# Optimization experiments

Hardware: AMD Instinct MI355X
Metric: run time of the kernel (lower is better)

## Reference

```python
import jax, jax.numpy as jnp
import numpy as np

B, T, D, H, V = 16, 256, 256, 512, 32000  # batch, seq_len, input_dim, hidden, vocab


def setup_inputs() -> dict:
    key = jax.random.key(0)
    ks = jax.random.split(key, 9)
    g = lambda k, shape, scale: (jax.random.normal(k, shape, jnp.float32) * scale)
    return {
        "images": g(ks[0], (B, D), 1.0),
        "labels": jax.random.randint(ks[1], (T, B), 0, V, dtype=jnp.int64),
        "embed_table": g(ks[2], (V, D), 0.02),
        "W_ih": g(ks[3], (4 * H, D), 1.0 / np.sqrt(H)),
        "W_hh": g(ks[4], (4 * H, H), 1.0 / np.sqrt(H)),
        "b_ih": g(ks[5], (4 * H,), 0.01),
        "b_hh": g(ks[6], (4 * H,), 0.01),
        "W_fc": g(ks[7], (V, H), 1.0 / np.sqrt(H)),
        "b_fc": g(ks[8], (V,), 0.01),
    }


def reference(images, labels, embed_table, W_ih, W_hh, b_ih, b_hh, W_fc, b_fc):
    # labels: (T, B) -> embedded (T, B, D); t=0 consumes images instead
    lab_emb = embed_table[labels]                               # (T, B, D)
    x_seq = jnp.concatenate([images[None], lab_emb[1:]], 0)     # (T, B, D)
    # precompute input-side gate contributions for all timesteps (one big GEMM)
    x_gates = jnp.einsum("tbd,gd->tbg", x_seq, W_ih) + b_ih + b_hh  # (T, B, 4H)

    hidden = W_hh.shape[1]
    bsz = images.shape[0]

    def step(carry, xg):
        h, c = carry
        gates = xg + h @ W_hh.T                                 # (B, 4H)
        i, f, g_, o = jnp.split(gates, 4, axis=-1)
        c = jax.nn.sigmoid(f) * c + jax.nn.sigmoid(i) * jnp.tanh(g_)
        h = jax.nn.sigmoid(o) * jnp.tanh(c)
        return (h, c), h

    init = (jnp.zeros((bsz, hidden), x_gates.dtype),
            jnp.zeros((bsz, hidden), x_gates.dtype))
    _, hs = jax.lax.scan(step, init, x_gates)                   # hs: (T, B, H)
    # fc_out applied to every timestep's hidden state
    return jnp.einsum("tbh,vh->tbv", hs, W_fc) + b_fc           # (T, B, V)
```

## Files before the change

kernel.cpp:

```cpp
#include <hip/hip_runtime.h>

typedef __attribute__((ext_vector_type(8))) short short8;
typedef __attribute__((ext_vector_type(4))) float f32x4;
typedef unsigned int uint;
typedef unsigned short ushort;

#define T_ 256
#define B_ 16
#define D_ 256
#define H_ 512
#define V_ 32000
#define GH 2048

__device__ __forceinline__ ushort f2bf(float f) {
    uint u = __float_as_uint(f);
    u += 0x7FFFu + ((u >> 16) & 1u);
    return (ushort)(u >> 16);
}

__device__ __forceinline__ float fsig(float x) {
    return 1.0f / (1.0f + __expf(-x));
}

__device__ __forceinline__ float ftanh(float x) {
    float a = __expf(-2.0f * fabsf(x));
    float t = (1.0f - a) / (1.0f + a);
    return x >= 0.0f ? t : -t;
}

__device__ __forceinline__ void cvt4(const float* s, ushort* d) {
    float4 v = *(const float4*)s;
    ushort4 o;
    o.x = f2bf(v.x); o.y = f2bf(v.y); o.z = f2bf(v.z); o.w = f2bf(v.w);
    *(ushort4*)d = o;
}

__global__ void prep_convert(const float* __restrict__ Wih, const float* __restrict__ Whh,
                             const float* __restrict__ Wfc, const float* __restrict__ bih,
                             const float* __restrict__ bhh,
                             ushort* __restrict__ dWih, ushort* __restrict__ dWhh,
                             ushort* __restrict__ dWfc, float* __restrict__ bsum) {
    const long nA = (long)GH * D_ / 4;
    const long nB = (long)GH * H_ / 4;
    const long nC = (long)V_ * H_ / 4;
    const long nS = GH / 4;
    long i = (long)blockIdx.x * blockDim.x + threadIdx.x;
    if (i >= nA + nB + nC + nS) return;
    if (i < nA) {
        cvt4(Wih + i * 4, dWih + i * 4);
    } else if (i < nA + nB) {
        long j = i - nA;
        cvt4(Whh + j * 4, dWhh + j * 4);
    } else if (i < nA + nB + nC) {
        long j = i - nA - nB;
        cvt4(Wfc + j * 4, dWfc + j * 4);
    } else {
        long j = (i - nA - nB - nC) * 4;
        float4 a = *(const float4*)(bih + j);
        float4 b = *(const float4*)(bhh + j);
        float4 o;
        o.x = a.x + b.x; o.y = a.y + b.y; o.z = a.z + b.z; o.w = a.w + b.w;
        *(float4*)(bsum + j) = o;
    }
}

__global__ void prep_xseq(const float* __restrict__ images, const int* __restrict__ labels,
                          const float* __restrict__ embed, ushort* __restrict__ xseq) {
    int m = blockIdx.x;
    int l = threadIdx.x;
    int t = m >> 4, b = m & 15;
    const float* src = (t == 0) ? (images + b * D_) : (embed + (long)labels[m] * D_);
    cvt4(src + l * 4, xseq + (long)m * D_ + l * 4);
}

template <int K>
__global__ __launch_bounds__(256) void gemm_bt(const ushort* __restrict__ A,
                                               const ushort* __restrict__ Bw,
                                               float* __restrict__ C,
                                               const float* __restrict__ bias,
                                               int ldc) {
    __shared__ ushort As[128 * 64];
    __shared__ ushort Bs[128 * 64];
    const int tid = threadIdx.x;
    const int lane = tid & 63;
    const int w = tid >> 6;
    const int wr = w >> 1, wc = w & 1;
    const long mBase = (long)blockIdx.x * 128;
    const long nBase = (long)blockIdx.y * 128;

    f32x4 acc[4][4];
#pragma unroll
    for (int i = 0; i < 4; ++i)
#pragma unroll
        for (int j = 0; j < 4; ++j) acc[i][j] = (f32x4){0.f, 0.f, 0.f, 0.f};

    const char* Ab = (const char*)A;
    const char* Bb = (const char*)Bw;

    for (int kk = 0; kk < K / 64; ++kk) {
#pragma unroll
        for (int it = 0; it < 4; ++it) {
            int c = w * 4 + it;
            int r = c * 8 + (lane >> 3);
            int sg = (lane & 7) ^ (r & 7);
            long aoff = (mBase + r) * (long)(K * 2) + kk * 128 + sg * 16;
            long boff = (nBase + r) * (long)(K * 2) + kk * 128 + sg * 16;
            __builtin_amdgcn_global_load_lds(
                (const __attribute__((address_space(1))) void*)(Ab + aoff),
                (__attribute__((address_space(3))) void*)((char*)As + c * 1024), 16, 0, 0);
            __builtin_amdgcn_global_load_lds(
                (const __attribute__((address_space(1))) void*)(Bb + boff),
                (__attribute__((address_space(3))) void*)((char*)Bs + c * 1024), 16, 0, 0);
        }
        __syncthreads();
#pragma unroll
        for (int k2 = 0; k2 < 2; ++k2) {
            short8 af[4], bfr[4];
#pragma unroll
            for (int mi = 0; mi < 4; ++mi) {
                int mrow = wr * 64 + mi * 16 + (lane & 15);
                int g = (k2 * 4 + (lane >> 4)) ^ (mrow & 7);
                af[mi] = *(const short8*)((const char*)As + mrow * 128 + g * 16);
            }
#pragma unroll
            for (int ni = 0; ni < 4; ++ni) {
                int nrow = wc * 64 + ni * 16 + (lane & 15);
                int g = (k2 * 4 + (lane >> 4)) ^ (nrow & 7);
                bfr[ni] = *(const short8*)((const char*)Bs + nrow * 128 + g * 16);
            }
#pragma unroll
            for (int mi = 0; mi < 4; ++mi)
#pragma unroll
                for (int ni = 0; ni < 4; ++ni)
                    acc[mi][ni] = __builtin_amdgcn_mfma_f32_16x16x32_bf16(
                        af[mi], bfr[ni], acc[mi][ni], 0, 0, 0);
        }
        __syncthreads();
    }
#pragma unroll
    for (int ni = 0; ni < 4; ++ni) {
        long col = nBase + wc * 64 + ni * 16 + (lane & 15);
        float bv = bias[col];
#pragma unroll
        for (int mi = 0; mi < 4; ++mi) {
            long row0 = mBase + wr * 64 + mi * 16 + ((lane >> 4) << 2);
#pragma unroll
            for (int rr = 0; rr < 4; ++rr)
                C[(row0 + rr) * (long)ldc + col] = acc[mi][ni][rr] + bv;
        }
    }
}

__global__ __launch_bounds__(256) void lstm_scan(const ushort* __restrict__ Whh,
                                                 const float* __restrict__ xg,
                                                 ushort* __restrict__ hs,
                                                 uint* __restrict__ flags) {
    __shared__ ushort Ws[64 * 512];
    __shared__ ushort hb[16 * 512];
    __shared__ float gb[4][16][16];
    __shared__ ushort hloc[16][16];

    const int tid = threadIdx.x;
    const int lane = tid & 63;
    const int w = tid >> 6;
    const int g = blockIdx.x;

#pragma unroll
    for (int j = 0; j < 16; ++j) {
        int gid = j * 256 + tid;
        int row = gid >> 6;
        int gcol = gid & 63;
        int srow = (row >> 4) * H_ + g * 16 + (row & 15);
        uint4 v = *(const uint4*)(Whh + (long)srow * H_ + gcol * 8);
        int dg = gcol ^ (row & 7);
        *(uint4*)((char*)Ws + row * 1024 + dg * 16) = v;
    }
    __syncthreads();

    const int b = tid >> 4;
    const int jj = tid & 15;
    float cst = 0.0f;

    for (int t = 0; t < T_; ++t) {
        long xb = ((long)t * B_ + b) * GH + g * 16 + jj;
        float gi = xg[xb];
        float gf = xg[xb + 512];
        float gg = xg[xb + 1024];
        float go = xg[xb + 1536];

        if (t > 0) {
            int fi = lane & 31;
            uint v = __hip_atomic_load(&flags[fi], __ATOMIC_RELAXED, __HIP_MEMORY_SCOPE_AGENT);
            int guard = 0;
            while (v < (uint)t) {
                __builtin_amdgcn_s_sleep(1);
                v = __hip_atomic_load(&flags[fi], __ATOMIC_RELAXED, __HIP_MEMORY_SCOPE_AGENT);
                if (++guard > (1 << 20)) break;
            }
            const uint* hsrcU = (const uint*)hs + ((long)(t - 1) * (B_ * H_)) / 2;
            const int row = tid >> 4;
            const int c0 = tid & 15;
            uint vals[16];
#pragma unroll
            for (int j2 = 0; j2 < 16; ++j2)
                vals[j2] = __hip_atomic_load((uint*)(hsrcU + row * 256 + c0 + j2 * 16),
                                             __ATOMIC_RELAXED, __HIP_MEMORY_SCOPE_AGENT);
#pragma unroll
            for (int j2 = 0; j2 < 16; ++j2) {
                int u = c0 + j2 * 16;
                int gcol = u >> 2, sub = u & 3;
                int dg = gcol ^ (row & 7);
                *(uint*)((char*)hb + row * 1024 + dg * 16 + sub * 4) = vals[j2];
            }
            __syncthreads();
            f32x4 acc0 = (f32x4){0.f, 0.f, 0.f, 0.f};
            f32x4 acc1 = (f32x4){0.f, 0.f, 0.f, 0.f};
            const int arow = lane & 15;
            const int brow = w * 16 + (lane & 15);
#pragma unroll
            for (int k0 = 0; k0 < 16; k0 += 2) {
                int ga0 = (k0 * 4 + (lane >> 4)) ^ (arow & 7);
                int gB0 = (k0 * 4 + (lane >> 4)) ^ (brow & 7);
                int ga1 = ((k0 + 1) * 4 + (lane >> 4)) ^ (arow & 7);
                int gB1 = ((k0 + 1) * 4 + (lane >> 4)) ^ (brow & 7);
                short8 a0 = *(const short8*)((const char*)hb + arow * 1024 + ga0 * 16);
                short8 b0 = *(const short8*)((const char*)Ws + brow * 1024 + gB0 * 16);
                short8 a1 = *(const short8*)((const char*)hb + arow * 1024 + ga1 * 16);
                short8 b1 = *(const short8*)((const char*)Ws + brow * 1024 + gB1 * 16);
                acc0 = __builtin_amdgcn_mfma_f32_16x16x32_bf16(a0, b0, acc0, 0, 0, 0);
                acc1 = __builtin_amdgcn_mfma_f32_16x16x32_bf16(a1, b1, acc1, 0, 0, 0);
            }
#pragma unroll
            for (int r = 0; r < 4; ++r)
                gb[w][((lane >> 4) << 2) + r][lane & 15] = acc0[r] + acc1[r];
            __syncthreads();
            gi += gb[0][b][jj];
            gf += gb[1][b][jj];
            gg += gb[2][b][jj];
            go += gb[3][b][jj];
        }
        float ii = fsig(gi), ff = fsig(gf), oo = fsig(go), tg = ftanh(gg);
        cst = ff * cst + ii * tg;
        float hv = oo * ftanh(cst);
        hloc[b][jj] = f2bf(hv);
        __syncthreads();
        if (tid < 128) {
            int bb = tid >> 3, u = tid & 7;
            uint val = (uint)hloc[bb][u * 2] | ((uint)hloc[bb][u * 2 + 1] << 16);
            uint* dst = (uint*)hs + (((long)t * B_ + bb) * H_ + g * 16) / 2 + u;
            __hip_atomic_store(dst, val, __ATOMIC_RELAXED, __HIP_MEMORY_SCOPE_AGENT);
        }
        asm volatile("s_waitcnt vmcnt(0)" ::: "memory");
        __syncthreads();
        if (tid == 0)
            __hip_atomic_store(&flags[g], (uint)(t + 1), __ATOMIC_RELAXED, __HIP_MEMORY_SCOPE_AGENT);
    }
}

extern "C" void kernel_launch(void* const* d_in, const int* in_sizes, int n_in,
                              void* d_out, int out_size, void* d_ws, size_t ws_size,
                              hipStream_t stream) {
    const float* images = (const float*)d_in[0];
    const int* labels   = (const int*)d_in[1];
    const float* embed  = (const float*)d_in[2];
    const float* Wih    = (const float*)d_in[3];
    const float* Whh    = (const float*)d_in[4];
    const float* bih    = (const float*)d_in[5];
    const float* bhh    = (const float*)d_in[6];
    const float* Wfc    = (const float*)d_in[7];
    const float* bfc    = (const float*)d_in[8];
    float* out = (float*)d_out;

    char* p = (char*)d_ws;
    ushort* dWfc = (ushort*)p; p += (long)V_ * H_ * 2;
    ushort* dWih = (ushort*)p; p += (long)GH * D_ * 2;
    ushort* dWhh = (ushort*)p; p += (long)GH * H_ * 2;
    ushort* xseq = (ushort*)p; p += (long)T_ * B_ * D_ * 2;
    float* xg    = (float*)p;  p += (long)T_ * B_ * GH * 4;
    ushort* hs   = (ushort*)p; p += (long)T_ * B_ * H_ * 2;
    float* bsum  = (float*)p;  p += GH * 4;
    uint* flags  = (uint*)p;   p += 256;

    hipMemsetAsync(flags, 0, 32 * sizeof(uint), stream);

    {
        long total = (long)GH * D_ / 4 + (long)GH * H_ / 4 + (long)V_ * H_ / 4 + GH / 4;
        int blocks = (int)((total + 255) / 256);
        prep_convert<<<blocks, 256, 0, stream>>>(Wih, Whh, Wfc, bih, bhh, dWih, dWhh, dWfc, bsum);
    }
    prep_xseq<<<T_ * B_, 64, 0, stream>>>(images, labels, embed, xseq);

    gemm_bt<D_><<<dim3(32, 16), 256, 0, stream>>>(xseq, dWih, xg, bsum, GH);

    lstm_scan<<<32, 256, 0, stream>>>(dWhh, xg, hs, flags);

    gemm_bt<H_><<<dim3(32, 250), 256, 0, stream>>>(hs, dWfc, out, bfc, V_);
}
```

Baseline: 1.031 ms.

## Replace per-step flag barrier with sentinel-valued hidden-state polling

The inter-block flag array is replaced by pre-filling the hidden-state buffer with a 0xFFFFFFFF sentinel. Each block now polls the previous step's h values directly until none are sentinel, and takes its own slice from shared memory. Writers store packed bf16 pairs straight from registers via a lane shuffle, which removes the vmcnt wait, one __syncthreads and the flag store on each step. This shortens the per-step serial critical path of the 256-step recurrence. The cost is a 4 MB memset, and correctness relies on no real bf16 pair ever equalling the sentinel, which holds because 0xFFFF is a NaN pattern.

New measurement: 897.4 us. -12.9%, faster.

```diff
diff --git a/kernel.cpp b/kernel.cpp
--- a/kernel.cpp
+++ b/kernel.cpp
@@ -11,6 +11,7 @@
 #define H_ 512
 #define V_ 32000
 #define GH 2048
+#define SENT 0xFFFFFFFFu
 
 __device__ __forceinline__ ushort f2bf(float f) {
     uint u = __float_as_uint(f);
@@ -153,8 +154,7 @@
 
 __global__ __launch_bounds__(256) void lstm_scan(const ushort* __restrict__ Whh,
                                                  const float* __restrict__ xg,
-                                                 ushort* __restrict__ hs,
-                                                 uint* __restrict__ flags) {
+                                                 ushort* __restrict__ hs) {
     __shared__ ushort Ws[64 * 512];
     __shared__ ushort hb[16 * 512];
     __shared__ float gb[4][16][16];
@@ -179,6 +179,8 @@
 
     const int b = tid >> 4;
     const int jj = tid & 15;
+    const int row = tid >> 4;
+    const int c0 = tid & 15;
     float cst = 0.0f;
 
     for (int t = 0; t < T_; ++t) {
@@ -189,28 +191,36 @@
         float go = xg[xb + 1536];
 
         if (t > 0) {
-            int fi = lane & 31;
-            uint v = __hip_atomic_load(&flags[fi], __ATOMIC_RELAXED, __HIP_MEMORY_SCOPE_AGENT);
+            uint vals[16];
+#pragma unroll
+            for (int j = 0; j < 16; ++j) {
+                int u = c0 + j * 16;
+                if ((u >> 3) == g)
+                    vals[j] = (uint)hloc[row][(u & 7) * 2] |
+                              ((uint)hloc[row][(u & 7) * 2 + 1] << 16);
+                else
+                    vals[j] = SENT;
+            }
+            uint* hsrcU = (uint*)hs + ((long)(t - 1) * (B_ * H_)) / 2 + row * 256;
             int guard = 0;
-            while (v < (uint)t) {
-                __builtin_amdgcn_s_sleep(1);
-                v = __hip_atomic_load(&flags[fi], __ATOMIC_RELAXED, __HIP_MEMORY_SCOPE_AGENT);
-                if (++guard > (1 << 20)) break;
-            }
-            const uint* hsrcU = (const uint*)hs + ((long)(t - 1) * (B_ * H_)) / 2;
-            const int row = tid >> 4;
-            const int c0 = tid & 15;
-            uint vals[16];
-#pragma unroll
-            for (int j2 = 0; j2 < 16; ++j2)
-                vals[j2] = __hip_atomic_load((uint*)(hsrcU + row * 256 + c0 + j2 * 16),
-                                             __ATOMIC_RELAXED, __HIP_MEMORY_SCOPE_AGENT);
-#pragma unroll
-            for (int j2 = 0; j2 < 16; ++j2) {
-                int u = c0 + j2 * 16;
+            for (;;) {
+                int pend = 0;
+#pragma unroll
+                for (int j = 0; j < 16; ++j) {
+                    if (vals[j] == SENT)
+                        vals[j] = __hip_atomic_load(hsrcU + c0 + j * 16,
+                                                    __ATOMIC_RELAXED, __HIP_MEMORY_SCOPE_AGENT);
+                }
+#pragma unroll
+                for (int j = 0; j < 16; ++j) pend += (vals[j] == SENT) ? 1 : 0;
+                if (pend == 0 || ++guard > (1 << 20)) break;
+            }
+#pragma unroll
+            for (int j = 0; j < 16; ++j) {
+                int u = c0 + j * 16;
                 int gcol = u >> 2, sub = u & 3;
                 int dg = gcol ^ (row & 7);
-                *(uint*)((char*)hb + row * 1024 + dg * 16 + sub * 4) = vals[j2];
+                *(uint*)((char*)hb + row * 1024 + dg * 16 + sub * 4) = vals[j];
             }
             __syncthreads();
             f32x4 acc0 = (f32x4){0.f, 0.f, 0.f, 0.f};
@@ -242,18 +252,16 @@
         float ii = fsig(gi), ff = fsig(gf), oo = fsig(go), tg = ftanh(gg);
         cst = ff * cst + ii * tg;
         float hv = oo * ftanh(cst);
-        hloc[b][jj] = f2bf(hv);
+        ushort hb16 = f2bf(hv);
+        hloc[b][jj] = hb16;
+        uint mybits = (uint)hb16;
+        uint partner = (uint)__shfl_xor((int)mybits, 1);
+        if ((jj & 1) == 0) {
+            uint val = mybits | (partner << 16);
+            uint* dst = (uint*)hs + ((long)t * B_ + b) * (H_ / 2) + (g * 16 + jj) / 2;
+            __hip_atomic_store(dst, val, __ATOMIC_RELAXED, __HIP_MEMORY_SCOPE_AGENT);
+        }
         __syncthreads();
-        if (tid < 128) {
-            int bb = tid >> 3, u = tid & 7;
-            uint val = (uint)hloc[bb][u * 2] | ((uint)hloc[bb][u * 2 + 1] << 16);
-            uint* dst = (uint*)hs + (((long)t * B_ + bb) * H_ + g * 16) / 2 + u;
-            __hip_atomic_store(dst, val, __ATOMIC_RELAXED, __HIP_MEMORY_SCOPE_AGENT);
-        }
-        asm volatile("s_waitcnt vmcnt(0)" ::: "memory");
-        __syncthreads();
-        if (tid == 0)
-            __hip_atomic_store(&flags[g], (uint)(t + 1), __ATOMIC_RELAXED, __HIP_MEMORY_SCOPE_AGENT);
     }
 }
 
@@ -279,9 +287,8 @@
     float* xg    = (float*)p;  p += (long)T_ * B_ * GH * 4;
     ushort* hs   = (ushort*)p; p += (long)T_ * B_ * H_ * 2;
     float* bsum  = (float*)p;  p += GH * 4;
-    uint* flags  = (uint*)p;   p += 256;
-
-    hipMemsetAsync(flags, 0, 32 * sizeof(uint), stream);
+
+    hipMemsetAsync(hs, 0xFF, (size_t)T_ * B_ * H_ * 2, stream);
 
     {
         long total = (long)GH * D_ / 4 + (long)GH * H_ / 4 + (long)V_ * H_ / 4 + GH / 4;
@@ -292,7 +299,7 @@
 
     gemm_bt<D_><<<dim3(32, 16), 256, 0, stream>>>(xseq, dWih, xg, bsum, GH);
 
-    lstm_scan<<<32, 256, 0, stream>>>(dWhh, xg, hs, flags);
+    lstm_scan<<<32, 256, 0, stream>>>(dWhh, xg, hs);
 
     gemm_bt<H_><<<dim3(32, 250), 256, 0, stream>>>(hs, dWfc, out, bfc, V_);
 }
```
